# Performance work log

Hardware: AMD Instinct MI355X
Metric: run time of the kernel (lower is better)

## Reference

```python
import jax, jax.numpy as jnp
import numpy as np

# Model dims (mamba_ssm defaults: expand=2, d_state=16, d_conv=4, dt_rank=ceil(d_model/16))
V, D_MODEL, N_LAYERS = 32000, 768, 2
D_INNER, D_STATE, D_CONV, DT_RANK = 1536, 16, 4, 48
BATCH, SEQ = 2, 2048


def setup_inputs() -> dict:
    key = jax.random.key(0)
    ks = jax.random.split(key, 10)

    def nrm(k, shape, s=0.02):
        return (jax.random.normal(k, shape) * s).astype(jnp.float32)

    x = jax.random.randint(ks[0], (BATCH, SEQ), 0, V)
    emb = nrm(ks[1], (V, D_MODEL))
    # per-layer Mamba params, stacked on leading layer axis
    W_in = nrm(ks[2], (N_LAYERS, 2 * D_INNER, D_MODEL))          # in_proj (no bias)
    conv_w = nrm(ks[3], (N_LAYERS, D_INNER, 1, D_CONV), 0.1)      # depthwise causal conv
    conv_b = jnp.zeros((N_LAYERS, D_INNER), jnp.float32)
    W_x = nrm(ks[4], (N_LAYERS, DT_RANK + 2 * D_STATE, D_INNER))  # x_proj (no bias)
    W_dt = nrm(ks[5], (N_LAYERS, D_INNER, DT_RANK), 0.05)         # dt_proj
    b_dt = jnp.full((N_LAYERS, D_INNER), -4.0, jnp.float32)       # softplus(-4) ~ small dt
    # A initialized as -exp(A_log) with A_log = log(1..d_state), per mamba_ssm
    A_log = jnp.log(jnp.broadcast_to(
        jnp.arange(1, D_STATE + 1, dtype=jnp.float32), (N_LAYERS, D_INNER, D_STATE)))
    D_skip = jnp.ones((N_LAYERS, D_INNER), jnp.float32)
    W_out = nrm(ks[6], (N_LAYERS, D_MODEL, D_INNER))              # out_proj (no bias)
    ln_g = jnp.ones((D_MODEL,), jnp.float32)
    ln_b = jnp.zeros((D_MODEL,), jnp.float32)
    head_w = nrm(ks[7], (V, D_MODEL))
    head_b = jnp.zeros((V,), jnp.float32)
    return dict(x=x, emb=emb, W_in=W_in, conv_w=conv_w, conv_b=conv_b, W_x=W_x,
                W_dt=W_dt, b_dt=b_dt, A_log=A_log, D_skip=D_skip, W_out=W_out,
                ln_g=ln_g, ln_b=ln_b, head_w=head_w, head_b=head_b)


def mamba_block(h, W_in, conv_w, conv_b, W_x, W_dt, b_dt, A_log, D_skip, W_out):
    # h: (B, L, D_MODEL)
    xz = jnp.einsum('bld,ed->ble', h, W_in)              # (B, L, 2*d_inner)
    u, z = jnp.split(xz, 2, axis=-1)
    # causal depthwise conv over time
    uc = jnp.transpose(u, (0, 2, 1))                     # (B, d_inner, L)
    uc = jax.lax.conv_general_dilated(
        uc, conv_w, window_strides=(1,), padding=[(D_CONV - 1, 0)],
        feature_group_count=D_INNER, dimension_numbers=('NCH', 'OIH', 'NCH'))
    u = jax.nn.silu(jnp.transpose(uc, (0, 2, 1)) + conv_b)
    # input-dependent dt, B, C
    x_dbl = jnp.einsum('bld,ed->ble', u, W_x)            # (B, L, dt_rank+2*d_state)
    dtl, Bm, Cm = jnp.split(x_dbl, [DT_RANK, DT_RANK + D_STATE], axis=-1)
    dt = jax.nn.softplus(jnp.einsum('blr,dr->bld', dtl, W_dt) + b_dt)  # (B, L, d_inner)
    A = -jnp.exp(A_log)                                  # (d_inner, d_state)

    def step(hst, inp):
        dt_t, u_t, B_t, C_t = inp                        # (B,d_inner),(B,d_inner),(B,d_state),(B,d_state)
        hst = jnp.exp(dt_t[..., None] * A) * hst + (dt_t * u_t)[..., None] * B_t[:, None, :]
        y_t = jnp.einsum('bds,bs->bd', hst, C_t)
        return hst, y_t

    h0 = jnp.zeros((u.shape[0], D_INNER, D_STATE), u.dtype)
    xs = (dt.transpose(1, 0, 2), u.transpose(1, 0, 2),
          Bm.transpose(1, 0, 2), Cm.transpose(1, 0, 2))
    _, ys = jax.lax.scan(step, h0, xs)                   # (L, B, d_inner)
    y = ys.transpose(1, 0, 2) + u * D_skip
    y = y * jax.nn.silu(z)
    return jnp.einsum('bli,oi->blo', y, W_out)           # back to (B, L, D_MODEL)


def reference(x, emb, W_in, conv_w, conv_b, W_x, W_dt, b_dt, A_log, D_skip,
              W_out, ln_g, ln_b, head_w, head_b):
    h = emb[x]                                           # (B, L, D_MODEL)
    for l in range(N_LAYERS):
        h = h + mamba_block(h, W_in[l], conv_w[l], conv_b[l], W_x[l], W_dt[l],
                            b_dt[l], A_log[l], D_skip[l], W_out[l])
    mu = jnp.mean(h, axis=-1, keepdims=True)
    var = jnp.mean((h - mu) ** 2, axis=-1, keepdims=True)
    hn = (h - mu) * jax.lax.rsqrt(var + 1e-5) * ln_g + ln_b
    return jnp.einsum('bld,vd->blv', hn, head_w) + head_b
```

## Files before the change

kernel.cpp:

```cpp
#include <hip/hip_runtime.h>
#include <hip/hip_bf16.h>
#include <stdint.h>

#define BL    4096
#define DM    768
#define DI    1536
#define DS    16
#define DCONV 4
#define DTR   48
#define NL    2
#define SEQL  2048
#define BATCH 2
#define VOC   32000
#define NCH   32
#define CT    64

typedef __bf16 bf16_t;
typedef __bf16 bf16x8 __attribute__((ext_vector_type(8)));
typedef __bf16 bf16x4 __attribute__((ext_vector_type(4)));
typedef float  f32x4  __attribute__((ext_vector_type(4)));

__device__ __forceinline__ float sigmoidf_(float x) { return 1.f / (1.f + __expf(-x)); }

__global__ __launch_bounds__(256) void k_embed(const int* __restrict__ x,
                                               const float* __restrict__ emb,
                                               float* __restrict__ h) {
  int row = blockIdx.x;
  int tok = x[row];
  const float* e = emb + (size_t)tok * DM;
  float* hr = h + (size_t)row * DM;
  for (int c = threadIdx.x; c < DM; c += 256) hr[c] = e[c];
}

__global__ __launch_bounds__(256) void k_cvt(const float* __restrict__ src,
                                             bf16_t* __restrict__ dst, long n4) {
  long i = (long)blockIdx.x * 256 + threadIdx.x;
  if (i >= n4) return;
  float4 v = ((const float4*)src)[i];
  bf16x4 o;
  o[0] = (bf16_t)v.x; o[1] = (bf16_t)v.y; o[2] = (bf16_t)v.z; o[3] = (bf16_t)v.w;
  ((bf16x4*)dst)[i] = o;
}

__global__ __launch_bounds__(256) void k_cvt_pad(const float* __restrict__ src,
                                                 bf16_t* __restrict__ dst,
                                                 int R, int C, int srcLd, int Cpad,
                                                 long total) {
  long i = (long)blockIdx.x * 256 + threadIdx.x;
  if (i >= total) return;
  int r = (int)(i / Cpad), c = (int)(i % Cpad);
  float v = (r < R && c < C) ? src[(size_t)r * srcLd + c] : 0.f;
  dst[i] = (bf16_t)v;
}

__global__ __launch_bounds__(256) void k_conv(const float* __restrict__ xz,
                                              const float* __restrict__ cw,
                                              const float* __restrict__ cb,
                                              float* __restrict__ uc, long total) {
  long i = (long)blockIdx.x * 256 + threadIdx.x;
  if (i >= total) return;
  int d = (int)(i % DI);
  long row = i / DI;
  int l = (int)(row % SEQL);
  const float* w = cw + (size_t)d * DCONV;
  float s = cb[d];
#pragma unroll
  for (int j = 0; j < DCONV; j++) {
    int lj = l - (DCONV - 1) + j;
    if (lj >= 0) s += xz[(row - (DCONV - 1) + j) * (2 * DI) + d] * w[j];
  }
  uc[i] = s * sigmoidf_(s);
}


__global__ __launch_bounds__(256) void k_scan1(const float* __restrict__ dt,
                                               const float* __restrict__ uc,
                                               const float* __restrict__ xdbl,
                                               const float* __restrict__ A_log,
                                               float* __restrict__ cA,
                                               float* __restrict__ cB) {
  int gi = blockIdx.x * 256 + threadIdx.x;
  int s = gi & 15;
  int rest = gi >> 4;
  int d = rest % DI;
  int rest2 = rest / DI;
  int c = rest2 % NCH;
  int b = rest2 / NCH;
  float a = -__expf(A_log[d * DS + s]);
  long l0 = (long)c * CT;
  const float* dtp = dt + ((long)b * SEQL + l0) * DI + d;
  const float* ucp = uc + ((long)b * SEQL + l0) * DI + d;
  const float* Bp  = xdbl + ((long)b * SEQL + l0) * 80 + DTR + s;
  float S = 0.f, hh = 0.f;
#pragma unroll 4
  for (int l = 0; l < CT; l++) {
    float dtv = dtp[(long)l * DI];
    float uv  = ucp[(long)l * DI];
    float Bv  = Bp[(long)l * 80];
    S += dtv;
    hh = __expf(dtv * a) * hh + (dtv * uv) * Bv;
  }
  cA[gi] = __expf(a * S);
  cB[gi] = hh;
}

__global__ __launch_bounds__(256) void k_scan2(const float* __restrict__ cA,
                                               const float* __restrict__ cB,
                                               float* __restrict__ hst) {
  int gj = blockIdx.x * 256 + threadIdx.x;
  int ds_ = gj & (DI * DS - 1);
  int b = gj / (DI * DS);
  float h = 0.f;
#pragma unroll
  for (int c = 0; c < NCH; c++) {
    long idx = ((long)(b * NCH + c) * DI * DS) + ds_;
    hst[idx] = h;
    h = cA[idx] * h + cB[idx];
  }
}

__global__ __launch_bounds__(256) void k_scan3(const float* __restrict__ dt,
                                               const float* __restrict__ uc,
                                               const float* __restrict__ xdbl,
                                               const float* __restrict__ A_log,
                                               const float* __restrict__ hst,
                                               float* __restrict__ ys) {
  int gi = blockIdx.x * 256 + threadIdx.x;
  int s = gi & 15;
  int rest = gi >> 4;
  int d = rest % DI;
  int rest2 = rest / DI;
  int c = rest2 % NCH;
  int b = rest2 / NCH;
  float a = -__expf(A_log[d * DS + s]);
  long l0 = (long)c * CT;
  const float* dtp = dt + ((long)b * SEQL + l0) * DI + d;
  const float* ucp = uc + ((long)b * SEQL + l0) * DI + d;
  const float* Bp  = xdbl + ((long)b * SEQL + l0) * 80 + DTR + s;
  const float* Cp  = Bp + DS;
  float* yp = ys + ((long)b * SEQL + l0) * DI + d;
  float h = hst[gi];
#pragma unroll 4
  for (int l = 0; l < CT; l++) {
    float dtv = dtp[(long)l * DI];
    float uv  = ucp[(long)l * DI];
    float Bv  = Bp[(long)l * 80];
    float Cv  = Cp[(long)l * 80];
    h = __expf(dtv * a) * h + (dtv * uv) * Bv;
    float y = h * Cv;
    y += __shfl_xor(y, 1);
    y += __shfl_xor(y, 2);
    y += __shfl_xor(y, 4);
    y += __shfl_xor(y, 8);
    if (s == 0) yp[(long)l * DI] = y;
  }
}

__global__ __launch_bounds__(256) void k_gate(const float* __restrict__ ys,
                                              const float* __restrict__ uc,
                                              const float* __restrict__ xz,
                                              const float* __restrict__ Dsk,
                                              bf16_t* __restrict__ o, long total) {
  long i = (long)blockIdx.x * 256 + threadIdx.x;
  if (i >= total) return;
  int d = (int)(i % DI);
  long row = i / DI;
  float y = ys[i] + uc[i] * Dsk[d];
  float z = xz[row * (2 * DI) + DI + d];
  o[i] = (bf16_t)(y * z * sigmoidf_(z));
}

__global__ __launch_bounds__(256) void k_ln(const float* __restrict__ h,
                                            const float* __restrict__ g,
                                            const float* __restrict__ bta,
                                            bf16_t* __restrict__ o) {
  __shared__ float sm[4];
  int row = blockIdx.x;
  int t = threadIdx.x;
  const float* hr = h + (long)row * DM;
  float v0 = hr[t], v1 = hr[t + 256], v2 = hr[t + 512];
  float s = v0 + v1 + v2;
#pragma unroll
  for (int off = 32; off > 0; off >>= 1) s += __shfl_down(s, off);
  if ((t & 63) == 0) sm[t >> 6] = s;
  __syncthreads();
  float mu = (sm[0] + sm[1] + sm[2] + sm[3]) * (1.f / DM);
  __syncthreads();
  float d0 = v0 - mu, d1 = v1 - mu, d2 = v2 - mu;
  float q = d0 * d0 + d1 * d1 + d2 * d2;
#pragma unroll
  for (int off = 32; off > 0; off >>= 1) q += __shfl_down(q, off);
  if ((t & 63) == 0) sm[t >> 6] = q;
  __syncthreads();
  float var = (sm[0] + sm[1] + sm[2] + sm[3]) * (1.f / DM);
  float rs = rsqrtf(var + 1e-5f);
  bf16_t* orow = o + (long)row * DM;
  orow[t]       = (bf16_t)(d0 * rs * g[t]       + bta[t]);
  orow[t + 256] = (bf16_t)(d1 * rs * g[t + 256] + bta[t + 256]);
  orow[t + 512] = (bf16_t)(d2 * rs * g[t + 512] + bta[t + 512]);
}

__device__ __forceinline__ void stage16(const bf16_t* gp, bf16_t* lp) {
  __builtin_amdgcn_global_load_lds(
      (const __attribute__((address_space(1))) uint32_t*)gp,
      (__attribute__((address_space(3))) uint32_t*)lp, 16, 0, 0);
}

template <int EPI>
__global__ __launch_bounds__(256) void k_gemm(const bf16_t* __restrict__ A,
                                              const bf16_t* __restrict__ W,
                                              float* __restrict__ C,
                                              const float* __restrict__ bias,
                                              int M, int N, int K, int ldc) {
  __shared__ bf16_t lA[128 * 32];
  __shared__ bf16_t lB[128 * 32];
  const int tid = threadIdx.x;
  const int lane = tid & 63;
  const int wv = tid >> 6;
  const int wm = wv >> 1, wn = wv & 1;
  const long m0 = (long)blockIdx.y * 128;
  const long n0 = (long)blockIdx.x * 128;
  const int r0 = tid >> 2;
  const int c8 = (tid & 3) * 8;
  const int fr = lane & 15;
  const int kq = lane >> 4;

  f32x4 acc[4][4];
#pragma unroll
  for (int i = 0; i < 4; i++)
#pragma unroll
    for (int j = 0; j < 4; j++) acc[i][j] = (f32x4){0.f, 0.f, 0.f, 0.f};

  const bf16_t* Ab = A + (m0 + r0) * (long)K + c8;
  const bf16_t* Wb = W + (n0 + r0) * (long)K + c8;
  bf16_t* lAp = lA + r0 * 32 + c8;
  bf16_t* lBp = lB + r0 * 32 + c8;
  const long s64K = 64L * K;

  for (int k0 = 0; k0 < K; k0 += 32) {
    __syncthreads();
    stage16(Ab + k0, lAp);
    stage16(Ab + k0 + s64K, lAp + 64 * 32);
    stage16(Wb + k0, lBp);
    stage16(Wb + k0 + s64K, lBp + 64 * 32);
    __syncthreads();
    bf16x8 af[4], bfv[4];
#pragma unroll
    for (int f = 0; f < 4; f++)
      af[f] = *(const bf16x8*)&lA[(wm * 64 + f * 16 + fr) * 32 + kq * 8];
#pragma unroll
    for (int f = 0; f < 4; f++)
      bfv[f] = *(const bf16x8*)&lB[(wn * 64 + f * 16 + fr) * 32 + kq * 8];
#pragma unroll
    for (int fm = 0; fm < 4; fm++)
#pragma unroll
      for (int fn = 0; fn < 4; fn++)
        acc[fm][fn] = __builtin_amdgcn_mfma_f32_16x16x32_bf16(af[fm], bfv[fn],
                                                              acc[fm][fn], 0, 0, 0);
  }

  const int r4 = (lane >> 4) * 4;
  const int cc = lane & 15;
#pragma unroll
  for (int fm = 0; fm < 4; fm++) {
    long rowb = m0 + wm * 64 + fm * 16 + r4;
#pragma unroll
    for (int fn = 0; fn < 4; fn++) {
      long col = n0 + wn * 64 + fn * 16 + cc;
      if (col < N) {
        float bv = (EPI == 1 || EPI == 3) ? bias[col] : 0.f;
#pragma unroll
        for (int r = 0; r < 4; r++) {
          long row = rowb + r;
          float v = acc[fm][fn][r];
          if (EPI == 1) v += bv;
          else if (EPI == 3) { v += bv; v = (v > 20.f) ? v : log1pf(__expf(v)); }
          else if (EPI == 2) v += C[row * (long)ldc + col];
          C[row * (long)ldc + col] = v;
        }
      }
    }
  }
}

static inline int cdiv_l(long a, long b) { return (int)((a + b - 1) / b); }

extern "C" void kernel_launch(void* const* d_in, const int* in_sizes, int n_in,
                              void* d_out, int out_size, void* d_ws, size_t ws_size,
                              hipStream_t stream) {
  (void)in_sizes; (void)n_in; (void)out_size; (void)ws_size;
  const int*   x      = (const int*)  d_in[0];
  const float* emb    = (const float*)d_in[1];
  const float* W_in   = (const float*)d_in[2];
  const float* conv_w = (const float*)d_in[3];
  const float* conv_b = (const float*)d_in[4];
  const float* W_x    = (const float*)d_in[5];
  const float* W_dt   = (const float*)d_in[6];
  const float* b_dt   = (const float*)d_in[7];
  const float* A_log  = (const float*)d_in[8];
  const float* D_skip = (const float*)d_in[9];
  const float* W_out  = (const float*)d_in[10];
  const float* ln_g   = (const float*)d_in[11];
  const float* ln_b   = (const float*)d_in[12];
  const float* head_w = (const float*)d_in[13];
  const float* head_b = (const float*)d_in[14];
  float* out = (float*)d_out;

  char* ws = (char*)d_ws;
  bf16_t* abuf = (bf16_t*)ws;
  bf16_t* wbuf = (bf16_t*)(ws + (size_t)BL * DI * 2);

  float* xz   = out;
  float* uc   = xz   + (size_t)BL * 2 * DI;
  float* xdbl = uc   + (size_t)BL * DI;
  float* dtb  = xdbl + (size_t)BL * 80;
  float* ysb  = dtb  + (size_t)BL * DI;
  float* h    = ysb  + (size_t)BL * DI;
  float* cA   = h    + (size_t)BL * DM;
  float* cB   = cA   + (size_t)BATCH * NCH * DI * DS;
  float* hst  = cB   + (size_t)BATCH * NCH * DI * DS;

  const int scan_blocks = BATCH * NCH * DI * DS / 256;
  const int st_blocks   = BATCH * DI * DS / 256;

  k_embed<<<BL, 256, 0, stream>>>(x, emb, h);

  for (int l = 0; l < NL; ++l) {
    k_cvt<<<cdiv_l((long)BL * DM / 4, 256), 256, 0, stream>>>(h, abuf, (long)BL * DM / 4);
    k_cvt<<<cdiv_l((long)2 * DI * DM / 4, 256), 256, 0, stream>>>(
        W_in + (size_t)l * 2 * DI * DM, wbuf, (long)2 * DI * DM / 4);
    k_gemm<0><<<dim3(2 * DI / 128, BL / 128), 256, 0, stream>>>(
        abuf, wbuf, xz, nullptr, BL, 2 * DI, DM, 2 * DI);
    k_conv<<<cdiv_l((long)BL * DI, 256), 256, 0, stream>>>(
        xz, conv_w + (size_t)l * DI * DCONV, conv_b + (size_t)l * DI, uc, (long)BL * DI);
    k_cvt<<<cdiv_l((long)BL * DI / 4, 256), 256, 0, stream>>>(uc, abuf, (long)BL * DI / 4);
    k_cvt_pad<<<cdiv_l(128L * DI, 256), 256, 0, stream>>>(
        W_x + (size_t)l * 80 * DI, wbuf, 80, DI, DI, DI, 128L * DI);
    k_gemm<0><<<dim3(1, BL / 128), 256, 0, stream>>>(
        abuf, wbuf, xdbl, nullptr, BL, 80, DI, 80);
    k_cvt_pad<<<cdiv_l((long)BL * 64, 256), 256, 0, stream>>>(
        xdbl, abuf, BL, DTR, 80, 64, (long)BL * 64);
    k_cvt_pad<<<cdiv_l((long)DI * 64, 256), 256, 0, stream>>>(
        W_dt + (size_t)l * DI * DTR, wbuf, DI, DTR, DTR, 64, (long)DI * 64);
    k_gemm<3><<<dim3(DI / 128, BL / 128), 256, 0, stream>>>(
        abuf, wbuf, dtb, b_dt + (size_t)l * DI, BL, DI, 64, DI);
    k_scan1<<<scan_blocks, 256, 0, stream>>>(dtb, uc, xdbl,
                                             A_log + (size_t)l * DI * DS, cA, cB);
    k_scan2<<<st_blocks, 256, 0, stream>>>(cA, cB, hst);
    k_scan3<<<scan_blocks, 256, 0, stream>>>(dtb, uc, xdbl,
                                             A_log + (size_t)l * DI * DS, hst, ysb);
    k_gate<<<cdiv_l((long)BL * DI, 256), 256, 0, stream>>>(
        ysb, uc, xz, D_skip + (size_t)l * DI, abuf, (long)BL * DI);
    k_cvt<<<cdiv_l((long)DM * DI / 4, 256), 256, 0, stream>>>(
        W_out + (size_t)l * DM * DI, wbuf, (long)DM * DI / 4);
    k_gemm<2><<<dim3(DM / 128, BL / 128), 256, 0, stream>>>(
        abuf, wbuf, h, nullptr, BL, DM, DI, DM);
  }

  k_ln<<<BL, 256, 0, stream>>>(h, ln_g, ln_b, abuf);
  k_cvt<<<cdiv_l((long)VOC * DM / 4, 256), 256, 0, stream>>>(head_w, wbuf, (long)VOC * DM / 4);
  k_gemm<1><<<dim3(VOC / 128, BL / 128), 256, 0, stream>>>(
      abuf, wbuf, out, head_b, BL, VOC, DM, VOC);
}
```

Measured before the change: 1.123 ms.

## Add 256x256 tiled bf16 GEMM with direct-to-LDS loads for in_proj and head

```diff
diff --git a/kernel.cpp b/kernel.cpp
--- a/kernel.cpp
+++ b/kernel.cpp
@@ -71,7 +71,6 @@
   }
   uc[i] = s * sigmoidf_(s);
 }
-
 
 __global__ __launch_bounds__(256) void k_scan1(const float* __restrict__ dt,
                                                const float* __restrict__ uc,
@@ -283,6 +282,121 @@
   }
 }
 
+
+#define GLD256(ab, j, ktt, pp) do {                                             \
+    int idx_ = (j) * 512 + tid;                                                 \
+    int r_ = idx_ >> 3; int c16_ = idx_ & 7;                                    \
+    size_t col_ = (size_t)(ktt) * 64 + (size_t)((c16_ ^ (r_ & 7)) << 3);        \
+    const bf16_t* gp_ = (ab) ? (Wp + ((size_t)(n0 + r_)) * K + col_)            \
+                             : (Ap + ((size_t)(m0 + r_)) * K + col_);           \
+    bf16_t* lp_ = lds + ((((pp) * 2 + (ab)) * 256 + r_) * 64) + c16_ * 8;       \
+    __builtin_amdgcn_global_load_lds(                                           \
+        (const __attribute__((address_space(1))) uint32_t*)gp_,                 \
+        (__attribute__((address_space(3))) uint32_t*)lp_, 16, 0, 0);            \
+  } while (0)
+
+#define STAGE2(pp, ktt, s) do {                                                 \
+    if ((s) == 0) { GLD256(0, 0, ktt, pp); GLD256(0, 2, ktt, pp); }             \
+    if ((s) == 1) { GLD256(1, 0, ktt, pp); GLD256(1, 1, ktt, pp); }             \
+    if ((s) == 2) { GLD256(1, 2, ktt, pp); GLD256(1, 3, ktt, pp); }             \
+    if ((s) == 3) { GLD256(0, 1, ktt, pp); GLD256(0, 3, ktt, pp); }             \
+  } while (0)
+
+#define COMPUTE256(pp, mg, kh) do {                                             \
+    const char* lb_ = (const char*)lds;                                         \
+    bf16x8 af_[4], bv_[4];                                                      \
+    _Pragma("unroll") for (int f = 0; f < 4; ++f) {                             \
+      int row_ = wm * 128 + (mg) * 64 + f * 16 + fr;                            \
+      int byte_ = (((pp) * 2 + 0) * 256 + row_) * 128 +                         \
+                  (((kh) * 64 + kq * 16) ^ ((row_ & 7) << 4));                  \
+      af_[f] = *(const bf16x8*)(lb_ + byte_);                                   \
+    }                                                                           \
+    _Pragma("unroll") for (int f = 0; f < 4; ++f) {                             \
+      int row_ = wn * 64 + f * 16 + fr;                                         \
+      int byte_ = (((pp) * 2 + 1) * 256 + row_) * 128 +                         \
+                  (((kh) * 64 + kq * 16) ^ ((row_ & 7) << 4));                  \
+      bv_[f] = *(const bf16x8*)(lb_ + byte_);                                   \
+    }                                                                           \
+    __builtin_amdgcn_s_setprio(1);                                              \
+    _Pragma("unroll") for (int fm = 0; fm < 4; ++fm)                            \
+      _Pragma("unroll") for (int fn = 0; fn < 4; ++fn)                          \
+        acc[(mg) * 4 + fm][fn] = __builtin_amdgcn_mfma_f32_16x16x32_bf16(       \
+            af_[fm], bv_[fn], acc[(mg) * 4 + fm][fn], 0, 0, 0);                 \
+    __builtin_amdgcn_s_setprio(0);                                              \
+  } while (0)
+
+#define WAITV2()  asm volatile("s_waitcnt vmcnt(2)" ::: "memory")
+#define WAITV0()  asm volatile("s_waitcnt vmcnt(0)" ::: "memory")
+#define BARRIER() do { __builtin_amdgcn_s_barrier();                            \
+                       asm volatile("" ::: "memory"); } while (0)
+
+template <int EPI>
+__global__ __launch_bounds__(512, 2) void k_gemm256(const bf16_t* __restrict__ Ap,
+                                                    const bf16_t* __restrict__ Wp,
+                                                    float* __restrict__ C,
+                                                    const float* __restrict__ bias,
+                                                    int K, int ldc, int nxtile) {
+  __shared__ bf16_t lds[2 * 2 * 256 * 64];
+  const int tid = threadIdx.x;
+  const int lane = tid & 63;
+  const int wid = tid >> 6;
+  const int wm = wid >> 2, wn = wid & 3;
+  const int fr = lane & 15, kq = lane >> 4;
+
+  const int cpx = gridDim.x >> 3;
+  const int wg = ((int)blockIdx.x & 7) * cpx + ((int)blockIdx.x >> 3);
+  const long m0 = (long)(wg / nxtile) * 256;
+  const long n0 = (long)(wg % nxtile) * 256;
+
+  f32x4 acc[8][4];
+#pragma unroll
+  for (int i = 0; i < 8; i++)
+#pragma unroll
+    for (int j = 0; j < 4; j++) acc[i][j] = (f32x4){0.f, 0.f, 0.f, 0.f};
+
+  STAGE2(0, 0, 0); STAGE2(0, 0, 1); STAGE2(0, 0, 2); STAGE2(0, 0, 3);
+  WAITV2();
+  BARRIER();
+
+  const int NT = K >> 6;
+  for (int kt = 0; kt < NT; ++kt) {
+    const int p = kt & 1;
+    const bool pre = (kt + 1 < NT);
+    if (pre) STAGE2(p ^ 1, kt + 1, 0);
+    COMPUTE256(p, 0, 0);
+    if (pre) WAITV2(); else WAITV0();
+    BARRIER();
+    if (pre) STAGE2(p ^ 1, kt + 1, 1);
+    COMPUTE256(p, 1, 0);
+    if (pre) STAGE2(p ^ 1, kt + 1, 2);
+    COMPUTE256(p, 0, 1);
+    if (pre) STAGE2(p ^ 1, kt + 1, 3);
+    COMPUTE256(p, 1, 1);
+    if (pre) {
+      WAITV2();
+      BARRIER();
+    }
+  }
+
+  const int r4 = (lane >> 4) * 4;
+  const int cc = lane & 15;
+#pragma unroll
+  for (int m = 0; m < 8; m++) {
+    long rowb = m0 + wm * 128 + (m >> 2) * 64 + (m & 3) * 16 + r4;
+#pragma unroll
+    for (int n = 0; n < 4; n++) {
+      long col = n0 + wn * 64 + n * 16 + cc;
+      float bv = (EPI == 1) ? bias[col] : 0.f;
+#pragma unroll
+      for (int r = 0; r < 4; r++) {
+        float v = acc[m][n][r];
+        if (EPI == 1) v += bv;
+        C[(rowb + r) * (long)ldc + col] = v;
+      }
+    }
+  }
+}
+
 static inline int cdiv_l(long a, long b) { return (int)((a + b - 1) / b); }
 
 extern "C" void kernel_launch(void* const* d_in, const int* in_sizes, int n_in,
@@ -329,8 +443,8 @@
     k_cvt<<<cdiv_l((long)BL * DM / 4, 256), 256, 0, stream>>>(h, abuf, (long)BL * DM / 4);
     k_cvt<<<cdiv_l((long)2 * DI * DM / 4, 256), 256, 0, stream>>>(
         W_in + (size_t)l * 2 * DI * DM, wbuf, (long)2 * DI * DM / 4);
-    k_gemm<0><<<dim3(2 * DI / 128, BL / 128), 256, 0, stream>>>(
-        abuf, wbuf, xz, nullptr, BL, 2 * DI, DM, 2 * DI);
+    k_gemm256<0><<<(BL / 256) * (2 * DI / 256), 512, 0, stream>>>(
+        abuf, wbuf, xz, nullptr, DM, 2 * DI, 2 * DI / 256);
     k_conv<<<cdiv_l((long)BL * DI, 256), 256, 0, stream>>>(
         xz, conv_w + (size_t)l * DI * DCONV, conv_b + (size_t)l * DI, uc, (long)BL * DI);
     k_cvt<<<cdiv_l((long)BL * DI / 4, 256), 256, 0, stream>>>(uc, abuf, (long)BL * DI / 4);
@@ -359,6 +473,6 @@
 
   k_ln<<<BL, 256, 0, stream>>>(h, ln_g, ln_b, abuf);
   k_cvt<<<cdiv_l((long)VOC * DM / 4, 256), 256, 0, stream>>>(head_w, wbuf, (long)VOC * DM / 4);
-  k_gemm<1><<<dim3(VOC / 128, BL / 128), 256, 0, stream>>>(
-      abuf, wbuf, out, head_b, BL, VOC, DM, VOC);
-}
+  k_gemm256<1><<<(BL / 256) * (VOC / 256), 512, 0, stream>>>(
+      abuf, wbuf, out, head_b, DM, VOC, VOC / 256);
+}
```

After: 1.016 ms. -9.5%, faster.
